# Optimization experiments

Hardware: AMD Instinct MI355X
Metric: run time of the kernel (lower is better)

The kernel has to match this reference:

```python
import jax, jax.numpy as jnp
import numpy as np
from jax import lax

B, H, W = 2, 256, 256
K = 7
K2 = K * K
IN_CH = 32 * 2 + 81  # 145


def _conv(x, w, b):
    y = lax.conv_general_dilated(x, w, (1, 1), 'SAME', dimension_numbers=('NCHW', 'OIHW', 'NCHW'))
    return y + b[None, :, None, None]


def _lrelu(x):
    return jnp.where(x >= 0, x, 0.1 * x)


def _predictor(x, w1, b1, w2, b2, w3, b3, wo, bo, ww, bw):
    f = _lrelu(_conv(x, w1, b1))
    f = _lrelu(_conv(f, w2, b2))
    f = _lrelu(_conv(f, w3, b3))
    offsets = _conv(f, wo, bo)                     # (B, 2*K2, H, W)
    weights = jax.nn.softmax(_conv(f, ww, bw), 1)  # (B, K2, H, W)
    return offsets, weights


def _sample(image, offsets, weights):
    b, c, h, w = image.shape
    k2 = weights.shape[1]
    off = offsets.reshape(b, k2, 2, h, w)
    dx, dy = off[:, :, 0], off[:, :, 1]
    gy, gx = jnp.meshgrid(jnp.arange(h, dtype=image.dtype), jnp.arange(w, dtype=image.dtype), indexing='ij')
    sx = gx[None, None] + dx  # (b,k2,h,w)
    sy = gy[None, None] + dy
    # Original normalizes with 2*s/(n-1)-1 (align_corners=True formula) but calls
    # grid_sample(align_corners=False): pixel coord = ((g+1)*n - 1)/2 = s*n/(n-1) - 0.5.
    # padding_mode='border' == clamp coord to [0, n-1] before bilinear.
    px = jnp.clip(sx * (w / (w - 1.0)) - 0.5, 0.0, w - 1.0)
    py = jnp.clip(sy * (h / (h - 1.0)) - 0.5, 0.0, h - 1.0)
    x0 = jnp.floor(px)
    y0 = jnp.floor(py)
    fx = (px - x0)[:, None]  # (b,1,k2,h,w)
    fy = (py - y0)[:, None]
    x0i = x0.astype(jnp.int32)
    y0i = y0.astype(jnp.int32)
    x1i = jnp.minimum(x0i + 1, w - 1)
    y1i = jnp.minimum(y0i + 1, h - 1)
    img = image.reshape(b, c, h * w)

    def gather(yi, xi):
        idx = (yi * w + xi).reshape(b, 1, k2 * h * w)
        return jnp.take_along_axis(img, idx, axis=2).reshape(b, c, k2, h, w)

    v00 = gather(y0i, x0i)
    v01 = gather(y0i, x1i)
    v10 = gather(y1i, x0i)
    v11 = gather(y1i, x1i)
    sampled = (v00 * (1 - fx) * (1 - fy) + v01 * fx * (1 - fy)
               + v10 * (1 - fx) * fy + v11 * fx * fy)
    return jnp.einsum('bkhw,bckhw->bchw', weights, sampled)


def setup_inputs() -> dict:
    key = jax.random.key(0)
    ks = iter(jax.random.split(key, 64))

    def nrm(shape, s=1.0):
        return jax.random.normal(next(ks), shape, jnp.float32) * s

    off0 = np.array([[j - K // 2, i - K // 2] for i in range(K) for j in range(K)],
                    np.float32).reshape(-1)  # interleaved (dx, dy) default grid

    def pred_params(p):
        return {
            p + '_w1': nrm((256, IN_CH, 3, 3), 0.02), p + '_b1': jnp.zeros((256,), jnp.float32),
            p + '_w2': nrm((256, 256, 3, 3), 0.02), p + '_b2': jnp.zeros((256,), jnp.float32),
            p + '_w3': nrm((128, 256, 3, 3), 0.02), p + '_b3': jnp.zeros((128,), jnp.float32),
            p + '_wo': nrm((2 * K2, 128, 3, 3), 0.01), p + '_bo': jnp.asarray(off0),
            p + '_ww': nrm((K2, 128, 3, 3), 0.02), p + '_bw': jnp.full((K2,), 1.0 / K2, jnp.float32),
        }

    inp = {
        'frame1': nrm((B, 3, H, W)),
        'frame2': nrm((B, 3, H, W)),
        'feat1': nrm((B, 32, H, W)),
        'feat2': nrm((B, 32, H, W)),
        'corr': nrm((B, 81, H, W)),
    }
    inp.update(pred_params('k1'))
    inp.update(pred_params('k2'))
    inp['bl_w1'] = nrm((64, IN_CH, 3, 3), 0.02)
    inp['bl_b1'] = jnp.zeros((64,), jnp.float32)
    inp['bl_w2'] = nrm((1, 64, 3, 3), 0.02)
    inp['bl_b2'] = jnp.zeros((1,), jnp.float32)
    return inp


def reference(frame1, frame2, feat1, feat2, corr,
              k1_w1, k1_b1, k1_w2, k1_b2, k1_w3, k1_b3, k1_wo, k1_bo, k1_ww, k1_bw,
              k2_w1, k2_b1, k2_w2, k2_b2, k2_w3, k2_b3, k2_wo, k2_bo, k2_ww, k2_bw,
              bl_w1, bl_b1, bl_w2, bl_b2):
    combined = jnp.concatenate([feat1, feat2, corr], axis=1)  # (B,145,H,W)
    off1, wt1 = _predictor(combined, k1_w1, k1_b1, k1_w2, k1_b2, k1_w3, k1_b3, k1_wo, k1_bo, k1_ww, k1_bw)
    off2, wt2 = _predictor(combined, k2_w1, k2_b1, k2_w2, k2_b2, k2_w3, k2_b3, k2_wo, k2_bo, k2_ww, k2_bw)
    s1 = _sample(frame1, off1, wt1)
    s2 = _sample(frame2, off2, wt2)
    blend = jax.nn.sigmoid(_conv(_lrelu(_conv(combined, bl_w1, bl_b1)), bl_w2, bl_b2))
    output = blend * s1 + (1.0 - blend) * s2
    return (output, blend, off1, off2, wt1, wt2)
```

## Files before the change

kernel.cpp:

```cpp
#include <hip/hip_runtime.h>


static constexpr int HW  = 65536;
static constexpr int WID = 256;
static constexpr int PAD = 66564;

using f32x16 = __attribute__((ext_vector_type(16))) float;
using f32x4  = __attribute__((ext_vector_type(4))) float;
using s16x8  = __attribute__((ext_vector_type(8))) short;

__device__ __forceinline__ unsigned short f2b(float f) {
    unsigned u = __builtin_bit_cast(unsigned, f);
    u += 0x7fffu + ((u >> 16) & 1u);
    return (unsigned short)(u >> 16);
}
__device__ __forceinline__ float b2f(unsigned short h) {
    unsigned u = ((unsigned)h) << 16;
    return __builtin_bit_cast(float, u);
}

template <int N> __device__ __forceinline__ void vm_wait() {
    asm volatile("s_waitcnt vmcnt(%0)" :: "n"(N) : "memory");
}

__global__ void pack_x(const float* __restrict__ feat1, const float* __restrict__ feat2,
                       const float* __restrict__ corr, unsigned short* __restrict__ Xc) {
    int idx = blockIdx.x * 256 + threadIdx.x;
    int g  = idx >> 17;
    int bp = idx & (2 * HW - 1);
    int b  = bp >> 16, p = bp & 65535;
    unsigned short v[8];
#pragma unroll
    for (int j = 0; j < 8; ++j) {
        int c = g * 8 + j;
        float val = 0.f;
        if (c < 32)       val = feat1[(size_t)(b * 32 + c) * HW + p];
        else if (c < 64)  val = feat2[(size_t)(b * 32 + (c - 32)) * HW + p];
        else if (c < 145) val = corr [(size_t)(b * 81 + (c - 64)) * HW + p];
        v[j] = f2b(val);
    }
    uint4 u;
    u.x = v[0] | ((unsigned)v[1] << 16);
    u.y = v[2] | ((unsigned)v[3] << 16);
    u.z = v[4] | ((unsigned)v[5] << 16);
    u.w = v[6] | ((unsigned)v[7] << 16);
    int y = p >> 8, x = p & 255;
    size_t cell = (size_t)b * PAD + (size_t)(y + 1) * 258 + (x + 1);
    *reinterpret_cast<uint4*>(Xc + cell * 160 + g * 8) = u;
}

__global__ void pack_w(const float* __restrict__ W, unsigned short* __restrict__ Wp,
                       int OC, int IC, int OCP, int KC) {
    int idx = blockIdx.x * 256 + threadIdx.x;
    int total = 9 * KC * 4 * OCP * 8;
    if (idx >= total) return;
    int i8 = idx & 7;  int r = idx >> 3;
    int oc = r % OCP;  r /= OCP;
    int g  = r & 3;    r >>= 2;
    int kb = r % KC;   int s = r / KC;
    int ic = kb * 32 + g * 8 + i8;
    float v = (oc < OC && ic < IC) ? W[((size_t)(oc * IC + ic)) * 9 + s] : 0.f;
    Wp[idx] = f2b(v);
}

__global__ void zero_border(unsigned short* __restrict__ buf, int C) {
    int idx = blockIdx.x * 256 + threadIdx.x;
    int G = C >> 3;
    int total = 2 * 1028 * G;
    if (idx >= total) return;
    int gi = idx % G; int r = idx / G;
    int ci = r % 1028; int b = r / 1028;
    int row, col;
    if (ci < 258)      { row = 0;            col = ci; }
    else if (ci < 516) { row = 257;          col = ci - 258; }
    else if (ci < 772) { row = ci - 516 + 1; col = 0; }
    else               { row = ci - 772 + 1; col = 257; }
    *reinterpret_cast<uint4*>(buf + ((size_t)b * PAD + row * 258 + col) * C + gi * 8) =
        make_uint4(0u, 0u, 0u, 0u);
}

template <int ICP, int OCF, int OCT, int MODE>
__global__ __launch_bounds__(256, 2) void conv3x3(
    const unsigned short* __restrict__ X,
    const uint4* __restrict__ Wp,
    const float* __restrict__ bias,
    unsigned short* __restrict__ outB,
    float* __restrict__ outF)
{
    constexpr int NT  = 256;
    constexpr int KC  = ICP / 32;
    constexpr int XGR = 1536;
    constexpr int WGR = 512;
    constexpr int XIT = XGR / NT;
    __shared__ uint4 lds[2 * XGR + 2 * WGR];

    const int t = threadIdx.x;
    const int lane = t & 63, wn = t >> 6;
    const int l31 = lane & 31, hi = lane >> 5;
    const int ocOff = blockIdx.y * 128;

    const int bid  = blockIdx.x;
    const int work = ((bid & 7) << 6) | (bid >> 3);
    const int bb = work >> 8;
    const int tt = work & 255;
    const int tr = tt >> 3, tc = tt & 7;

    auto stage_x = [&](int kb, int slot) {
#pragma unroll
        for (int it = 0; it < XIT; ++it) {
            int G = it * NT + t;
            int g = G / 384;
            int cell = G - g * 384;
            cell = min(cell, 339);
            int rr = cell / 34, cc = cell - rr * 34;
            const unsigned short* src = X +
                ((size_t)bb * PAD + (size_t)(tr * 8 + rr) * 258 + tc * 32 + cc) * ICP +
                kb * 32 + g * 8;
            __builtin_amdgcn_global_load_lds(
                (const __attribute__((address_space(1))) unsigned int*)src,
                (__attribute__((address_space(3))) unsigned int*)&lds[slot * XGR + it * NT + (t & ~63)],
                16, 0, 0);
        }
    };
    auto stage_w = [&](int s, int kb, int slot) {
#pragma unroll
        for (int it = 0; it < 2; ++it) {
            int G = it * NT + t;
            int g = G >> 7, oc = G & 127;
            const uint4* src = Wp + ((size_t)(s * KC + kb) * 4 + g) * OCF + ocOff + oc;
            __builtin_amdgcn_global_load_lds(
                (const __attribute__((address_space(1))) unsigned int*)src,
                (__attribute__((address_space(3))) unsigned int*)&lds[2 * XGR + slot * WGR + it * NT + (t & ~63)],
                16, 0, 0);
        }
    };

    f32x16 acc[4][2] = {};

    stage_x(0, 0);
    stage_w(0, 0, 0);
    vm_wait<0>();
    __builtin_amdgcn_s_barrier();

    int ph = 0;
    for (int kb = 0; kb < KC; ++kb) {
        const int xb = (kb & 1) * XGR;
#pragma unroll
        for (int s = 0; s < 9; ++s) {
            const int wcur = 2 * XGR + (ph & 1) * WGR;
            const bool lastPhase = (kb == KC - 1) && (s == 8);
            if (s < 8) {
                stage_w(s + 1, kb, (ph & 1) ^ 1);
            } else if (kb + 1 < KC) {
                stage_w(0, kb + 1, (ph & 1) ^ 1);
                stage_x(kb + 1, (kb & 1) ^ 1);
            }
            if (lastPhase)      vm_wait<0>();
            else if (s == 8)    vm_wait<2 + XIT>();
            else                vm_wait<2>();
            __builtin_amdgcn_s_barrier();

            const int dy = s / 3, dx = s - 3 * (s / 3);
            __builtin_amdgcn_s_setprio(1);
#pragma unroll
            for (int ks = 0; ks < 2; ++ks) {
                uint4 a[4], bq[2];
#pragma unroll
                for (int fm = 0; fm < 4; ++fm)
                    a[fm] = lds[wcur + (ks * 2 + hi) * 128 + fm * 32 + l31];
#pragma unroll
                for (int fn = 0; fn < 2; ++fn)
                    bq[fn] = lds[xb + (ks * 2 + hi) * 384 + (wn * 2 + fn + dy) * 34 + dx + l31];
#pragma unroll
                for (int fm = 0; fm < 4; ++fm)
#pragma unroll
                    for (int fn = 0; fn < 2; ++fn)
                        acc[fm][fn] = __builtin_amdgcn_mfma_f32_32x32x16_bf16(
                            __builtin_bit_cast(s16x8, a[fm]),
                            __builtin_bit_cast(s16x8, bq[fn]),
                            acc[fm][fn], 0, 0, 0);
            }
            __builtin_amdgcn_s_setprio(0);
            __builtin_amdgcn_s_barrier();
            ph ^= 1;
        }
    }

#pragma unroll
    for (int fm = 0; fm < 4; ++fm) {
#pragma unroll
        for (int fn = 0; fn < 2; ++fn) {
            const int prow = wn * 2 + fn;
            if (MODE == 0) {
                const size_t cellp = (size_t)bb * PAD + (size_t)(tr * 8 + prow + 1) * 258 + tc * 32 + l31 + 1;
#pragma unroll
                for (int q = 0; q < 4; ++q) {
                    const int goc = ocOff + fm * 32 + q * 8 + hi * 4;
                    if (goc < OCT) {
                        float4 bv = *reinterpret_cast<const float4*>(bias + goc);
                        const float* bvp = reinterpret_cast<const float*>(&bv);
                        unsigned short o[4];
#pragma unroll
                        for (int j = 0; j < 4; ++j) {
                            float r = acc[fm][fn][q * 4 + j] + bvp[j];
                            r = (r >= 0.f) ? r : 0.1f * r;
                            o[j] = f2b(r);
                        }
                        uint2 pk;
                        pk.x = o[0] | ((unsigned)o[1] << 16);
                        pk.y = o[2] | ((unsigned)o[3] << 16);
                        *reinterpret_cast<uint2*>(outB + cellp * OCT + goc) = pk;
                    }
                }
            } else {
                const int py = tr * 8 + prow, px = tc * 32 + l31;
#pragma unroll
                for (int q = 0; q < 4; ++q) {
#pragma unroll
                    for (int j = 0; j < 4; ++j) {
                        const int oc = ocOff + fm * 32 + q * 8 + hi * 4 + j;
                        if (oc < OCT)
                            outF[((size_t)bb * OCT + oc) * HW + py * WID + px] =
                                acc[fm][fn][q * 4 + j] + bias[oc];
                    }
                }
            }
        }
    }
}

__global__ void softmax49(float* __restrict__ L) {
    int idx = blockIdx.x * 256 + threadIdx.x;
    int b = idx >> 16, p = idx & 65535;
    float* lp = L + (size_t)b * 49 * HW + p;
    float v[49];
    float mx = -1e30f;
#pragma unroll
    for (int k = 0; k < 49; ++k) { v[k] = lp[(size_t)k * HW]; mx = fmaxf(mx, v[k]); }
    float sum = 0.f;
#pragma unroll
    for (int k = 0; k < 49; ++k) { v[k] = expf(v[k] - mx); sum += v[k]; }
    float inv = 1.f / sum;
#pragma unroll
    for (int k = 0; k < 49; ++k) lp[(size_t)k * HW] = v[k] * inv;
}

__global__ void blend2k(const unsigned short* __restrict__ Fb, const float* __restrict__ W2,
                        const float* __restrict__ B2, float* __restrict__ blendOut) {
    int idx = blockIdx.x * 256 + threadIdx.x;
    int b = idx >> 16, p = idx & 65535, y = p >> 8, x = p & 255;
    float acc = B2[0];
#pragma unroll
    for (int ry = 0; ry < 3; ++ry) {
#pragma unroll
        for (int rx = 0; rx < 3; ++rx) {
            const unsigned short* fp = Fb + ((size_t)b * PAD + (size_t)(y + ry) * 258 + (x + rx)) * 64;
#pragma unroll
            for (int g = 0; g < 8; ++g) {
                uint4 u = *reinterpret_cast<const uint4*>(fp + g * 8);
                unsigned w[4] = {u.x, u.y, u.z, u.w};
#pragma unroll
                for (int h = 0; h < 4; ++h) {
                    int c = g * 8 + h * 2;
                    acc += b2f((unsigned short)(w[h] & 0xffffu)) * W2[(c)     * 9 + ry * 3 + rx];
                    acc += b2f((unsigned short)(w[h] >> 16))     * W2[(c + 1) * 9 + ry * 3 + rx];
                }
            }
        }
    }
    blendOut[idx] = 1.f / (1.f + expf(-acc));
}

__global__ void pack_frames(const float* __restrict__ f1, const float* __restrict__ f2,
                            f32x4* __restrict__ Ff) {
    int idx = blockIdx.x * 256 + threadIdx.x;
    int fr = idx >> 17; int bp = idx & (2 * HW - 1);
    const float* src = fr ? f2 : f1;
    int b = bp >> 16, p = bp & 65535;
    f32x4 v;
    v[0] = src[(size_t)(b * 3 + 0) * HW + p];
    v[1] = src[(size_t)(b * 3 + 1) * HW + p];
    v[2] = src[(size_t)(b * 3 + 2) * HW + p];
    v[3] = 0.f;
    Ff[(size_t)fr * 2 * HW + bp] = v;
}

__device__ __forceinline__ void sample_accum4(const f32x4* __restrict__ img,
                                              const float* __restrict__ off,
                                              const float* __restrict__ wt,
                                              int x, int y, f32x4& s) {
    for (int k = 0; k < 49; ++k) {
        float dx = off[(size_t)(2 * k) * HW];
        float dy = off[(size_t)(2 * k + 1) * HW];
        float w  = wt [(size_t)k * HW];
        float px = ((float)x + dx) * (256.f / 255.f) - 0.5f;
        float py = ((float)y + dy) * (256.f / 255.f) - 0.5f;
        px = fminf(fmaxf(px, 0.f), 255.f);
        py = fminf(fmaxf(py, 0.f), 255.f);
        float x0f = floorf(px), y0f = floorf(py);
        float fx = px - x0f, fy = py - y0f;
        int x0 = (int)x0f, y0 = (int)y0f;
        int x1 = min(x0 + 1, 255), y1 = min(y0 + 1, 255);
        const f32x4* r0 = img + y0 * WID;
        const f32x4* r1 = img + y1 * WID;
        f32x4 v = (1.f - fy) * ((1.f - fx) * r0[x0] + fx * r0[x1]) +
                  fy         * ((1.f - fx) * r1[x0] + fx * r1[x1]);
        s += w * v;
    }
}

__global__ void sample_final(const f32x4* __restrict__ Ff,
                             const float* __restrict__ off1, const float* __restrict__ off2,
                             const float* __restrict__ wt1, const float* __restrict__ wt2,
                             const float* __restrict__ blend, float* __restrict__ out) {
    int idx = blockIdx.x * 256 + threadIdx.x;
    int b = idx >> 16, p = idx & 65535, y = p >> 8, x = p & 255;
    f32x4 s1 = {0.f, 0.f, 0.f, 0.f}, s2 = {0.f, 0.f, 0.f, 0.f};
    sample_accum4(Ff + (size_t)b * HW, off1 + (size_t)b * 98 * HW + p,
                  wt1 + (size_t)b * 49 * HW + p, x, y, s1);
    sample_accum4(Ff + (size_t)(2 + b) * HW, off2 + (size_t)b * 98 * HW + p,
                  wt2 + (size_t)b * 49 * HW + p, x, y, s2);
    float bl = blend[idx];
#pragma unroll
    for (int c = 0; c < 3; ++c)
        out[(size_t)(b * 3 + c) * HW + p] = bl * s1[c] + (1.f - bl) * s2[c];
}

extern "C" void kernel_launch(void* const* d_in, const int* in_sizes, int n_in,
                              void* d_out, int out_size, void* d_ws, size_t ws_size,
                              hipStream_t stream) {
    (void)in_sizes; (void)n_in; (void)out_size; (void)ws_size;
    const float* frame1 = (const float*)d_in[0];
    const float* frame2 = (const float*)d_in[1];
    const float* feat1  = (const float*)d_in[2];
    const float* feat2  = (const float*)d_in[3];
    const float* corr   = (const float*)d_in[4];
    const float* Wsrc[2][5];
    const float* Bsrc[2][5];
    for (int pdx = 0; pdx < 2; ++pdx) {
        int base = 5 + pdx * 10;
        for (int l = 0; l < 5; ++l) {
            Wsrc[pdx][l] = (const float*)d_in[base + 2 * l];
            Bsrc[pdx][l] = (const float*)d_in[base + 2 * l + 1];
        }
    }
    const float* bl_w1 = (const float*)d_in[25];
    const float* bl_b1 = (const float*)d_in[26];
    const float* bl_w2 = (const float*)d_in[27];
    const float* bl_b2 = (const float*)d_in[28];

    float* out      = (float*)d_out;
    float* out_bl   = out + 393216;
    float* out_off[2] = {out + 524288,   out + 13369344};
    float* out_wt [2] = {out + 26214400, out + 32636928};

    char* ws = (char*)d_ws;
    size_t o = 0;
    auto alloc = [&](size_t bytes) { char* p = ws + o; o += (bytes + 255) & ~(size_t)255; return p; };
    unsigned short* Xc   = (unsigned short*)alloc((size_t)2 * PAD * 160 * 2);
    unsigned short* bufA = (unsigned short*)alloc((size_t)2 * PAD * 256 * 2);
    unsigned short* bufB = (unsigned short*)alloc((size_t)2 * PAD * 256 * 2);
    unsigned short *WpC1[2], *WpC2[2], *WpC3[2], *WpCo[2], *WpCw[2];
    for (int pdx = 0; pdx < 2; ++pdx) {
        WpC1[pdx] = (unsigned short*)alloc((size_t)9 * 256 * 160 * 2);
        WpC2[pdx] = (unsigned short*)alloc((size_t)9 * 256 * 256 * 2);
        WpC3[pdx] = (unsigned short*)alloc((size_t)9 * 128 * 256 * 2);
        WpCo[pdx] = (unsigned short*)alloc((size_t)9 * 128 * 128 * 2);
        WpCw[pdx] = (unsigned short*)alloc((size_t)9 * 128 * 128 * 2);
    }
    unsigned short* WpBl = (unsigned short*)alloc((size_t)9 * 128 * 160 * 2);
    f32x4* Ff = (f32x4*)bufA;

    auto packw = [&](const float* W, unsigned short* Wp, int OC, int IC, int OCP, int ICP) {
        int total = 9 * OCP * ICP;
        pack_w<<<(total + 255) / 256, 256, 0, stream>>>(W, Wp, OC, IC, OCP, ICP / 32);
    };
    auto zb = [&](unsigned short* buf, int C) {
        int total = 2 * 1028 * (C / 8);
        zero_border<<<(total + 255) / 256, 256, 0, stream>>>(buf, C);
    };

    zb(Xc, 160);
    pack_x<<<(2 * HW * 20) / 256, 256, 0, stream>>>(feat1, feat2, corr, Xc);
    for (int pdx = 0; pdx < 2; ++pdx) {
        packw(Wsrc[pdx][0], WpC1[pdx], 256, 145, 256, 160);
        packw(Wsrc[pdx][1], WpC2[pdx], 256, 256, 256, 256);
        packw(Wsrc[pdx][2], WpC3[pdx], 128, 256, 128, 256);
        packw(Wsrc[pdx][3], WpCo[pdx],  98, 128, 128, 128);
        packw(Wsrc[pdx][4], WpCw[pdx],  49, 128, 128, 128);
    }
    packw(bl_w1, WpBl, 64, 145, 128, 160);
    zb(bufB, 256);

    for (int pdx = 0; pdx < 2; ++pdx) {
        zb(bufA, 256);
        conv3x3<160, 256, 256, 0><<<dim3(512, 2), 256, 0, stream>>>(
            Xc, (const uint4*)WpC1[pdx], Bsrc[pdx][0], bufA, nullptr);
        conv3x3<256, 256, 256, 0><<<dim3(512, 2), 256, 0, stream>>>(
            bufA, (const uint4*)WpC2[pdx], Bsrc[pdx][1], bufB, nullptr);
        zb(bufA, 128);
        conv3x3<256, 128, 128, 0><<<dim3(512, 1), 256, 0, stream>>>(
            bufB, (const uint4*)WpC3[pdx], Bsrc[pdx][2], bufA, nullptr);
        conv3x3<128, 128, 98, 1><<<dim3(512, 1), 256, 0, stream>>>(
            bufA, (const uint4*)WpCo[pdx], Bsrc[pdx][3], nullptr, out_off[pdx]);
        conv3x3<128, 128, 49, 1><<<dim3(512, 1), 256, 0, stream>>>(
            bufA, (const uint4*)WpCw[pdx], Bsrc[pdx][4], nullptr, out_wt[pdx]);
        softmax49<<<512, 256, 0, stream>>>(out_wt[pdx]);
    }

    zb(bufB, 64);
    conv3x3<160, 128, 64, 0><<<dim3(512, 1), 256, 0, stream>>>(
        Xc, (const uint4*)WpBl, bl_b1, bufB, nullptr);
    blend2k<<<512, 256, 0, stream>>>(bufB, bl_w2, bl_b2, out_bl);

    pack_frames<<<(4 * HW) / 256, 256, 0, stream>>>(frame1, frame2, Ff);
    sample_final<<<512, 256, 0, stream>>>(Ff, out_off[0], out_off[1],
                                          out_wt[0], out_wt[1], out_bl, out);
}
```

Baseline: 1.289 ms.

## Double conv tile height to 16 rows with 512-thread blocks and per-row weight staging

The conv3x3 kernel now uses 512-thread blocks (8 waves) covering a 16x32 pixel tile instead of 8x32, halving the grid, so each staged weight block is reused across twice as many pixels. Weights are staged three taps at a time (one kernel row dy per phase), which cuts the number of barriers per input-channel chunk from 18 to 6. LDS grows to 128 KB, which together with the larger block may limit how many blocks fit per CU and reduce latency hiding.

Measured after the change: 1.214 ms. 1.06x faster.

```diff
diff --git a/kernel.cpp b/kernel.cpp
--- a/kernel.cpp
+++ b/kernel.cpp
@@ -80,57 +80,53 @@
 }
 
 template <int ICP, int OCF, int OCT, int MODE>
-__global__ __launch_bounds__(256, 2) void conv3x3(
+__global__ __launch_bounds__(512, 2) void conv3x3(
     const unsigned short* __restrict__ X,
     const uint4* __restrict__ Wp,
     const float* __restrict__ bias,
     unsigned short* __restrict__ outB,
     float* __restrict__ outF)
 {
-    constexpr int NT  = 256;
-    constexpr int KC  = ICP / 32;
-    constexpr int XGR = 1536;
-    constexpr int WGR = 512;
-    constexpr int XIT = XGR / NT;
-    __shared__ uint4 lds[2 * XGR + 2 * WGR];
+    constexpr int KC = ICP / 32;
+    __shared__ uint4 lds[8192];
 
     const int t = threadIdx.x;
     const int lane = t & 63, wn = t >> 6;
     const int l31 = lane & 31, hi = lane >> 5;
     const int ocOff = blockIdx.y * 128;
 
-    const int bid  = blockIdx.x;
-    const int work = ((bid & 7) << 6) | (bid >> 3);
-    const int bb = work >> 8;
-    const int tt = work & 255;
+    const int bid = blockIdx.x;
+    const int q8  = gridDim.x >> 3;
+    const int work = (bid & 7) * q8 + (bid >> 3);
+    const int bb = work >> 7;
+    const int tt = work & 127;
     const int tr = tt >> 3, tc = tt & 7;
 
-    auto stage_x = [&](int kb, int slot) {
-#pragma unroll
-        for (int it = 0; it < XIT; ++it) {
-            int G = it * NT + t;
-            int g = G / 384;
-            int cell = G - g * 384;
-            cell = min(cell, 339);
+    auto stage_x = [&](int kb2, int slot) {
+#pragma unroll
+        for (int it = 0; it < 5; ++it) {
+            int G = it * 512 + t;
+            int g = G / 640;
+            int cell = G - g * 640;
+            cell = min(cell, 611);
             int rr = cell / 34, cc = cell - rr * 34;
             const unsigned short* src = X +
-                ((size_t)bb * PAD + (size_t)(tr * 8 + rr) * 258 + tc * 32 + cc) * ICP +
-                kb * 32 + g * 8;
+                ((size_t)bb * PAD + (size_t)(tr * 16 + rr) * 258 + tc * 32 + cc) * ICP +
+                kb2 * 32 + g * 8;
             __builtin_amdgcn_global_load_lds(
                 (const __attribute__((address_space(1))) unsigned int*)src,
-                (__attribute__((address_space(3))) unsigned int*)&lds[slot * XGR + it * NT + (t & ~63)],
+                (__attribute__((address_space(3))) unsigned int*)&lds[slot * 2560 + it * 512 + (t & ~63)],
                 16, 0, 0);
         }
     };
-    auto stage_w = [&](int s, int kb, int slot) {
-#pragma unroll
-        for (int it = 0; it < 2; ++it) {
-            int G = it * NT + t;
-            int g = G >> 7, oc = G & 127;
-            const uint4* src = Wp + ((size_t)(s * KC + kb) * 4 + g) * OCF + ocOff + oc;
+    auto stage_wg = [&](int kb2, int dy2, int wslot) {
+#pragma unroll
+        for (int j = 0; j < 3; ++j) {
+            int s = dy2 * 3 + j;
+            const uint4* src = Wp + ((size_t)(s * KC + kb2) * 4 + (t >> 7)) * OCF + ocOff + (t & 127);
             __builtin_amdgcn_global_load_lds(
                 (const __attribute__((address_space(1))) unsigned int*)src,
-                (__attribute__((address_space(3))) unsigned int*)&lds[2 * XGR + slot * WGR + it * NT + (t & ~63)],
+                (__attribute__((address_space(3))) unsigned int*)&lds[5120 + wslot * 1536 + j * 512 + (t & ~63)],
                 16, 0, 0);
         }
     };
@@ -138,49 +134,52 @@
     f32x16 acc[4][2] = {};
 
     stage_x(0, 0);
-    stage_w(0, 0, 0);
-    vm_wait<0>();
-    __builtin_amdgcn_s_barrier();
+    stage_wg(0, 0, 0);
 
     int ph = 0;
+#pragma unroll 1
     for (int kb = 0; kb < KC; ++kb) {
-        const int xb = (kb & 1) * XGR;
-#pragma unroll
-        for (int s = 0; s < 9; ++s) {
-            const int wcur = 2 * XGR + (ph & 1) * WGR;
-            const bool lastPhase = (kb == KC - 1) && (s == 8);
-            if (s < 8) {
-                stage_w(s + 1, kb, (ph & 1) ^ 1);
+        const int xb = (kb & 1) * 2560;
+#pragma unroll
+        for (int dy = 0; dy < 3; ++dy) {
+            const int wb = 5120 + (ph & 1) * 1536;
+            if (dy < 2) {
+                stage_wg(kb, dy + 1, (ph & 1) ^ 1);
+                vm_wait<3>();
             } else if (kb + 1 < KC) {
-                stage_w(0, kb + 1, (ph & 1) ^ 1);
+                stage_wg(kb + 1, 0, (ph & 1) ^ 1);
                 stage_x(kb + 1, (kb & 1) ^ 1);
+                vm_wait<8>();
+            } else {
+                vm_wait<0>();
             }
-            if (lastPhase)      vm_wait<0>();
-            else if (s == 8)    vm_wait<2 + XIT>();
-            else                vm_wait<2>();
             __builtin_amdgcn_s_barrier();
 
-            const int dy = s / 3, dx = s - 3 * (s / 3);
-            __builtin_amdgcn_s_setprio(1);
-#pragma unroll
-            for (int ks = 0; ks < 2; ++ks) {
-                uint4 a[4], bq[2];
-#pragma unroll
-                for (int fm = 0; fm < 4; ++fm)
-                    a[fm] = lds[wcur + (ks * 2 + hi) * 128 + fm * 32 + l31];
-#pragma unroll
-                for (int fn = 0; fn < 2; ++fn)
-                    bq[fn] = lds[xb + (ks * 2 + hi) * 384 + (wn * 2 + fn + dy) * 34 + dx + l31];
-#pragma unroll
-                for (int fm = 0; fm < 4; ++fm)
+#pragma unroll
+            for (int dxi = 0; dxi < 3; ++dxi) {
+                uint4 a[2][4], bq[2][2];
+#pragma unroll
+                for (int ks = 0; ks < 2; ++ks) {
+#pragma unroll
+                    for (int fm = 0; fm < 4; ++fm)
+                        a[ks][fm] = lds[wb + dxi * 512 + (ks * 2 + hi) * 128 + fm * 32 + l31];
 #pragma unroll
                     for (int fn = 0; fn < 2; ++fn)
-                        acc[fm][fn] = __builtin_amdgcn_mfma_f32_32x32x16_bf16(
-                            __builtin_bit_cast(s16x8, a[fm]),
-                            __builtin_bit_cast(s16x8, bq[fn]),
-                            acc[fm][fn], 0, 0, 0);
+                        bq[ks][fn] = lds[xb + (ks * 2 + hi) * 640 + (wn * 2 + fn + dy) * 34 + dxi + l31];
+                }
+                __builtin_amdgcn_s_setprio(1);
+#pragma unroll
+                for (int ks = 0; ks < 2; ++ks)
+#pragma unroll
+                    for (int fm = 0; fm < 4; ++fm)
+#pragma unroll
+                        for (int fn = 0; fn < 2; ++fn)
+                            acc[fm][fn] = __builtin_amdgcn_mfma_f32_32x32x16_bf16(
+                                __builtin_bit_cast(s16x8, a[ks][fm]),
+                                __builtin_bit_cast(s16x8, bq[ks][fn]),
+                                acc[fm][fn], 0, 0, 0);
+                __builtin_amdgcn_s_setprio(0);
             }
-            __builtin_amdgcn_s_setprio(0);
             __builtin_amdgcn_s_barrier();
             ph ^= 1;
         }
@@ -192,17 +191,17 @@
         for (int fn = 0; fn < 2; ++fn) {
             const int prow = wn * 2 + fn;
             if (MODE == 0) {
-                const size_t cellp = (size_t)bb * PAD + (size_t)(tr * 8 + prow + 1) * 258 + tc * 32 + l31 + 1;
-#pragma unroll
-                for (int q = 0; q < 4; ++q) {
-                    const int goc = ocOff + fm * 32 + q * 8 + hi * 4;
+                const size_t cellp = (size_t)bb * PAD + (size_t)(tr * 16 + prow + 1) * 258 + tc * 32 + l31 + 1;
+#pragma unroll
+                for (int qd = 0; qd < 4; ++qd) {
+                    const int goc = ocOff + fm * 32 + qd * 8 + hi * 4;
                     if (goc < OCT) {
                         float4 bv = *reinterpret_cast<const float4*>(bias + goc);
                         const float* bvp = reinterpret_cast<const float*>(&bv);
                         unsigned short o[4];
 #pragma unroll
                         for (int j = 0; j < 4; ++j) {
-                            float r = acc[fm][fn][q * 4 + j] + bvp[j];
+                            float r = acc[fm][fn][qd * 4 + j] + bvp[j];
                             r = (r >= 0.f) ? r : 0.1f * r;
                             o[j] = f2b(r);
                         }
@@ -213,15 +212,15 @@
                     }
                 }
             } else {
-                const int py = tr * 8 + prow, px = tc * 32 + l31;
-#pragma unroll
-                for (int q = 0; q < 4; ++q) {
+                const int py = tr * 16 + prow, px = tc * 32 + l31;
+#pragma unroll
+                for (int qd = 0; qd < 4; ++qd) {
 #pragma unroll
                     for (int j = 0; j < 4; ++j) {
-                        const int oc = ocOff + fm * 32 + q * 8 + hi * 4 + j;
+                        const int oc = ocOff + fm * 32 + qd * 8 + hi * 4 + j;
                         if (oc < OCT)
                             outF[((size_t)bb * OCT + oc) * HW + py * WID + px] =
-                                acc[fm][fn][q * 4 + j] + bias[oc];
+                                acc[fm][fn][qd * 4 + j] + bias[oc];
                     }
                 }
             }
@@ -394,22 +393,22 @@
 
     for (int pdx = 0; pdx < 2; ++pdx) {
         zb(bufA, 256);
-        conv3x3<160, 256, 256, 0><<<dim3(512, 2), 256, 0, stream>>>(
+        conv3x3<160, 256, 256, 0><<<dim3(256, 2), 512, 0, stream>>>(
             Xc, (const uint4*)WpC1[pdx], Bsrc[pdx][0], bufA, nullptr);
-        conv3x3<256, 256, 256, 0><<<dim3(512, 2), 256, 0, stream>>>(
+        conv3x3<256, 256, 256, 0><<<dim3(256, 2), 512, 0, stream>>>(
             bufA, (const uint4*)WpC2[pdx], Bsrc[pdx][1], bufB, nullptr);
         zb(bufA, 128);
-        conv3x3<256, 128, 128, 0><<<dim3(512, 1), 256, 0, stream>>>(
+        conv3x3<256, 128, 128, 0><<<dim3(256, 1), 512, 0, stream>>>(
             bufB, (const uint4*)WpC3[pdx], Bsrc[pdx][2], bufA, nullptr);
-        conv3x3<128, 128, 98, 1><<<dim3(512, 1), 256, 0, stream>>>(
+        conv3x3<128, 128, 98, 1><<<dim3(256, 1), 512, 0, stream>>>(
             bufA, (const uint4*)WpCo[pdx], Bsrc[pdx][3], nullptr, out_off[pdx]);
-        conv3x3<128, 128, 49, 1><<<dim3(512, 1), 256, 0, stream>>>(
+        conv3x3<128, 128, 49, 1><<<dim3(256, 1), 512, 0, stream>>>(
             bufA, (const uint4*)WpCw[pdx], Bsrc[pdx][4], nullptr, out_wt[pdx]);
         softmax49<<<512, 256, 0, stream>>>(out_wt[pdx]);
     }
 
     zb(bufB, 64);
-    conv3x3<160, 128, 64, 0><<<dim3(512, 1), 256, 0, stream>>>(
+    conv3x3<160, 128, 64, 0><<<dim3(256, 1), 512, 0, stream>>>(
         Xc, (const uint4*)WpBl, bl_b1, bufB, nullptr);
     blend2k<<<512, 256, 0, stream>>>(bufB, bl_w2, bl_b2, out_bl);
 
```

## Restructure conv3x3 into 512-thread blocks covering all output channels with 16x16 MFMA

Applied to the files above, without the earlier changes.

The implicit-GEMM conv kernel now uses 512 threads per block and covers the full output-channel width in one block, where before it split channels across grid.y. Each input tile is therefore staged once rather than once per channel half. The kernel switches from 32x32x16 to 16x16x32 bf16 MFMA with a 2x4 wave layout. Weights use triple buffering with prefetch two taps ahead, LDS fragments are read before the barrier, and input offsets are precomputed and incremented. The trade-off is higher register and LDS pressure per block, plus more complex wait-count bookkeeping.

After: 1.230 ms. 1.05x faster.

```diff
diff --git a/kernel.cpp b/kernel.cpp
--- a/kernel.cpp
+++ b/kernel.cpp
@@ -5,7 +5,6 @@
 static constexpr int WID = 256;
 static constexpr int PAD = 66564;
 
-using f32x16 = __attribute__((ext_vector_type(16))) float;
 using f32x4  = __attribute__((ext_vector_type(4))) float;
 using s16x8  = __attribute__((ext_vector_type(8))) short;
 
@@ -80,149 +79,160 @@
 }
 
 template <int ICP, int OCF, int OCT, int MODE>
-__global__ __launch_bounds__(256, 2) void conv3x3(
+__global__ __launch_bounds__(512, 2) void conv3x3(
     const unsigned short* __restrict__ X,
     const uint4* __restrict__ Wp,
     const float* __restrict__ bias,
     unsigned short* __restrict__ outB,
     float* __restrict__ outF)
 {
-    constexpr int NT  = 256;
     constexpr int KC  = ICP / 32;
-    constexpr int XGR = 1536;
-    constexpr int WGR = 512;
-    constexpr int XIT = XGR / NT;
-    __shared__ uint4 lds[2 * XGR + 2 * WGR];
+    constexpr int MF  = OCF / 32;
+    constexpr int WST = OCF / 128;
+    constexpr int WGR = OCF * 4;
+    __shared__ uint4 lds[3072 + 3 * WGR];
 
     const int t = threadIdx.x;
-    const int lane = t & 63, wn = t >> 6;
-    const int l31 = lane & 31, hi = lane >> 5;
-    const int ocOff = blockIdx.y * 128;
-
-    const int bid  = blockIdx.x;
+    const int lane = t & 63;
+    const int wv = t >> 6;
+    const int wm = wv >> 2, wn = wv & 3;
+    const int l15 = lane & 15, kq = lane >> 4;
+
+    const int bid = blockIdx.x;
     const int work = ((bid & 7) << 6) | (bid >> 3);
     const int bb = work >> 8;
     const int tt = work & 255;
     const int tr = tt >> 3, tc = tt & 7;
 
-    auto stage_x = [&](int kb, int slot) {
-#pragma unroll
-        for (int it = 0; it < XIT; ++it) {
-            int G = it * NT + t;
-            int g = G / 384;
-            int cell = G - g * 384;
-            cell = min(cell, 339);
-            int rr = cell / 34, cc = cell - rr * 34;
-            const unsigned short* src = X +
-                ((size_t)bb * PAD + (size_t)(tr * 8 + rr) * 258 + tc * 32 + cc) * ICP +
-                kb * 32 + g * 8;
-            __builtin_amdgcn_global_load_lds(
-                (const __attribute__((address_space(1))) unsigned int*)src,
-                (__attribute__((address_space(3))) unsigned int*)&lds[slot * XGR + it * NT + (t & ~63)],
-                16, 0, 0);
+    unsigned xoff[3];
+#pragma unroll
+    for (int it = 0; it < 3; ++it) {
+        int G = it * 512 + t;
+        int g = G / 384;
+        int cell = G - g * 384;
+        cell = min(cell, 339);
+        int rr = cell / 34, cc = cell - rr * 34;
+        xoff[it] = (unsigned)(((bb * PAD + (tr * 8 + rr) * 258 + tc * 32 + cc) * ICP
+                               + g * 8) * 2);
+    }
+    const int tdst = t & ~63;
+
+    auto gload = [&](const char* src, uint4* dst) {
+        __builtin_amdgcn_global_load_lds(
+            (const __attribute__((address_space(1))) unsigned int*)src,
+            (__attribute__((address_space(3))) unsigned int*)dst, 16, 0, 0);
+    };
+    auto stage_x = [&](int slot) {
+#pragma unroll
+        for (int it = 0; it < 3; ++it)
+            gload((const char*)X + xoff[it], &lds[slot * 1536 + it * 512 + tdst]);
+    };
+    auto stage_w = [&](int s2, int kb2, int slot) {
+        const unsigned base = (unsigned)(s2 * KC + kb2) * (unsigned)(WGR * 16);
+#pragma unroll
+        for (int it = 0; it < WST; ++it)
+            gload((const char*)Wp + base + (unsigned)((it * 512 + t) * 16),
+                  &lds[3072 + slot * WGR + it * 512 + tdst]);
+    };
+
+    const unsigned aLane = (unsigned)((kq * OCF + wm * (OCF / 2) + l15) * 16) + 49152u;
+    const unsigned bLane = (unsigned)((kq * 384 + wn * 68 + l15) * 16);
+    const char* ldsc = (const char*)lds;
+
+    f32x4 acc[MF][4] = {};
+
+    stage_x(0);
+    stage_w(0, 0, 0);
+    stage_w(1, 0, 1);
+    vm_wait<WST>();
+    __builtin_amdgcn_s_barrier();
+
+#pragma unroll 1
+    for (int kb = 0; kb < KC; ++kb) {
+        const unsigned bBase = bLane + (unsigned)((kb & 1) * 24576);
+#pragma unroll
+        for (int s = 0; s < 9; ++s) {
+            const int dy = s / 3, dx = s - 3 * (s / 3);
+            const unsigned aBase = aLane + (unsigned)((s % 3) * (WGR * 16));
+
+            uint4 aR[MF], bR[4];
+#pragma unroll
+            for (int fm = 0; fm < MF; ++fm)
+                aR[fm] = *(const uint4*)(ldsc + aBase + (unsigned)(fm * 256));
+#pragma unroll
+            for (int fn = 0; fn < 4; ++fn)
+                bR[fn] = *(const uint4*)(ldsc + bBase +
+                    (unsigned)(((((fn >> 1) + dy) * 34) + (fn & 1) * 16 + dx) * 16));
+
+            if (s < 7) {
+                stage_w(s + 2, kb, (s + 2) % 3);
+            } else if (kb + 1 < KC) {
+                stage_w(s - 7, kb + 1, (s + 2) % 3);
+            }
+            if (s == 0 && kb + 1 < KC) {
+#pragma unroll
+                for (int it = 0; it < 3; ++it) xoff[it] += 64u;
+                stage_x((kb + 1) & 1);
+            }
+
+            __builtin_amdgcn_s_barrier();
+            asm volatile("s_waitcnt lgkmcnt(0)" ::: "memory");
+            __builtin_amdgcn_sched_barrier(0);
+            __builtin_amdgcn_s_setprio(1);
+#pragma unroll
+            for (int fm = 0; fm < MF; ++fm)
+#pragma unroll
+                for (int fn = 0; fn < 4; ++fn)
+                    acc[fm][fn] = __builtin_amdgcn_mfma_f32_16x16x32_bf16(
+                        __builtin_bit_cast(s16x8, aR[fm]),
+                        __builtin_bit_cast(s16x8, bR[fn]),
+                        acc[fm][fn], 0, 0, 0);
+            __builtin_amdgcn_s_setprio(0);
+
+            if (s == 0) {
+                if (kb + 1 < KC) vm_wait<WST + 3>(); else vm_wait<WST>();
+            } else if (s < 7) {
+                vm_wait<WST>();
+            } else {
+                if (kb + 1 < KC) vm_wait<WST>(); else vm_wait<0>();
+            }
+            __builtin_amdgcn_s_barrier();
         }
-    };
-    auto stage_w = [&](int s, int kb, int slot) {
-#pragma unroll
-        for (int it = 0; it < 2; ++it) {
-            int G = it * NT + t;
-            int g = G >> 7, oc = G & 127;
-            const uint4* src = Wp + ((size_t)(s * KC + kb) * 4 + g) * OCF + ocOff + oc;
-            __builtin_amdgcn_global_load_lds(
-                (const __attribute__((address_space(1))) unsigned int*)src,
-                (__attribute__((address_space(3))) unsigned int*)&lds[2 * XGR + slot * WGR + it * NT + (t & ~63)],
-                16, 0, 0);
-        }
-    };
-
-    f32x16 acc[4][2] = {};
-
-    stage_x(0, 0);
-    stage_w(0, 0, 0);
-    vm_wait<0>();
-    __builtin_amdgcn_s_barrier();
-
-    int ph = 0;
-    for (int kb = 0; kb < KC; ++kb) {
-        const int xb = (kb & 1) * XGR;
-#pragma unroll
-        for (int s = 0; s < 9; ++s) {
-            const int wcur = 2 * XGR + (ph & 1) * WGR;
-            const bool lastPhase = (kb == KC - 1) && (s == 8);
-            if (s < 8) {
-                stage_w(s + 1, kb, (ph & 1) ^ 1);
-            } else if (kb + 1 < KC) {
-                stage_w(0, kb + 1, (ph & 1) ^ 1);
-                stage_x(kb + 1, (kb & 1) ^ 1);
-            }
-            if (lastPhase)      vm_wait<0>();
-            else if (s == 8)    vm_wait<2 + XIT>();
-            else                vm_wait<2>();
-            __builtin_amdgcn_s_barrier();
-
-            const int dy = s / 3, dx = s - 3 * (s / 3);
-            __builtin_amdgcn_s_setprio(1);
-#pragma unroll
-            for (int ks = 0; ks < 2; ++ks) {
-                uint4 a[4], bq[2];
-#pragma unroll
-                for (int fm = 0; fm < 4; ++fm)
-                    a[fm] = lds[wcur + (ks * 2 + hi) * 128 + fm * 32 + l31];
-#pragma unroll
-                for (int fn = 0; fn < 2; ++fn)
-                    bq[fn] = lds[xb + (ks * 2 + hi) * 384 + (wn * 2 + fn + dy) * 34 + dx + l31];
-#pragma unroll
-                for (int fm = 0; fm < 4; ++fm)
-#pragma unroll
-                    for (int fn = 0; fn < 2; ++fn)
-                        acc[fm][fn] = __builtin_amdgcn_mfma_f32_32x32x16_bf16(
-                            __builtin_bit_cast(s16x8, a[fm]),
-                            __builtin_bit_cast(s16x8, bq[fn]),
-                            acc[fm][fn], 0, 0, 0);
-            }
-            __builtin_amdgcn_s_setprio(0);
-            __builtin_amdgcn_s_barrier();
-            ph ^= 1;
-        }
-    }
-
-#pragma unroll
-    for (int fm = 0; fm < 4; ++fm) {
-#pragma unroll
-        for (int fn = 0; fn < 2; ++fn) {
-            const int prow = wn * 2 + fn;
+    }
+
+#pragma unroll
+    for (int fm = 0; fm < MF; ++fm) {
+#pragma unroll
+        for (int fn = 0; fn < 4; ++fn) {
+            const int prow = wn * 2 + (fn >> 1);
+            const int pcol = (fn & 1) * 16 + l15;
+            const int oc0 = wm * (OCF / 2) + fm * 16 + kq * 4;
             if (MODE == 0) {
-                const size_t cellp = (size_t)bb * PAD + (size_t)(tr * 8 + prow + 1) * 258 + tc * 32 + l31 + 1;
-#pragma unroll
-                for (int q = 0; q < 4; ++q) {
-                    const int goc = ocOff + fm * 32 + q * 8 + hi * 4;
-                    if (goc < OCT) {
-                        float4 bv = *reinterpret_cast<const float4*>(bias + goc);
-                        const float* bvp = reinterpret_cast<const float*>(&bv);
-                        unsigned short o[4];
-#pragma unroll
-                        for (int j = 0; j < 4; ++j) {
-                            float r = acc[fm][fn][q * 4 + j] + bvp[j];
-                            r = (r >= 0.f) ? r : 0.1f * r;
-                            o[j] = f2b(r);
-                        }
-                        uint2 pk;
-                        pk.x = o[0] | ((unsigned)o[1] << 16);
-                        pk.y = o[2] | ((unsigned)o[3] << 16);
-                        *reinterpret_cast<uint2*>(outB + cellp * OCT + goc) = pk;
+                if (oc0 < OCT) {
+                    const size_t cellp = (size_t)bb * PAD +
+                        (size_t)(tr * 8 + prow + 1) * 258 + tc * 32 + pcol + 1;
+                    float4 bv = *reinterpret_cast<const float4*>(bias + oc0);
+                    const float* bvp = reinterpret_cast<const float*>(&bv);
+                    unsigned short o[4];
+#pragma unroll
+                    for (int j = 0; j < 4; ++j) {
+                        float r = acc[fm][fn][j] + bvp[j];
+                        r = (r >= 0.f) ? r : 0.1f * r;
+                        o[j] = f2b(r);
                     }
+                    uint2 pk;
+                    pk.x = o[0] | ((unsigned)o[1] << 16);
+                    pk.y = o[2] | ((unsigned)o[3] << 16);
+                    *reinterpret_cast<uint2*>(outB + cellp * OCT + oc0) = pk;
                 }
             } else {
-                const int py = tr * 8 + prow, px = tc * 32 + l31;
-#pragma unroll
-                for (int q = 0; q < 4; ++q) {
-#pragma unroll
-                    for (int j = 0; j < 4; ++j) {
-                        const int oc = ocOff + fm * 32 + q * 8 + hi * 4 + j;
-                        if (oc < OCT)
-                            outF[((size_t)bb * OCT + oc) * HW + py * WID + px] =
-                                acc[fm][fn][q * 4 + j] + bias[oc];
-                    }
+                const int py = tr * 8 + prow, px = tc * 32 + pcol;
+#pragma unroll
+                for (int j = 0; j < 4; ++j) {
+                    const int oc = oc0 + j;
+                    if (oc < OCT)
+                        outF[((size_t)bb * OCT + oc) * HW + py * WID + px] =
+                            acc[fm][fn][j] + bias[oc];
                 }
             }
         }
@@ -394,22 +404,22 @@
 
     for (int pdx = 0; pdx < 2; ++pdx) {
         zb(bufA, 256);
-        conv3x3<160, 256, 256, 0><<<dim3(512, 2), 256, 0, stream>>>(
+        conv3x3<160, 256, 256, 0><<<512, 512, 0, stream>>>(
             Xc, (const uint4*)WpC1[pdx], Bsrc[pdx][0], bufA, nullptr);
-        conv3x3<256, 256, 256, 0><<<dim3(512, 2), 256, 0, stream>>>(
+        conv3x3<256, 256, 256, 0><<<512, 512, 0, stream>>>(
             bufA, (const uint4*)WpC2[pdx], Bsrc[pdx][1], bufB, nullptr);
         zb(bufA, 128);
-        conv3x3<256, 128, 128, 0><<<dim3(512, 1), 256, 0, stream>>>(
+        conv3x3<256, 128, 128, 0><<<512, 512, 0, stream>>>(
             bufB, (const uint4*)WpC3[pdx], Bsrc[pdx][2], bufA, nullptr);
-        conv3x3<128, 128, 98, 1><<<dim3(512, 1), 256, 0, stream>>>(
+        conv3x3<128, 128, 98, 1><<<512, 512, 0, stream>>>(
             bufA, (const uint4*)WpCo[pdx], Bsrc[pdx][3], nullptr, out_off[pdx]);
-        conv3x3<128, 128, 49, 1><<<dim3(512, 1), 256, 0, stream>>>(
+        conv3x3<128, 128, 49, 1><<<512, 512, 0, stream>>>(
             bufA, (const uint4*)WpCw[pdx], Bsrc[pdx][4], nullptr, out_wt[pdx]);
         softmax49<<<512, 256, 0, stream>>>(out_wt[pdx]);
     }
 
     zb(bufB, 64);
-    conv3x3<160, 128, 64, 0><<<dim3(512, 1), 256, 0, stream>>>(
+    conv3x3<160, 128, 64, 0><<<512, 512, 0, stream>>>(
         Xc, (const uint4*)WpBl, bl_b1, bufB, nullptr);
     blend2k<<<512, 256, 0, stream>>>(bufB, bl_w2, bl_b2, out_bl);
 
```
